# Kernel tuning notes

Hardware: AMD Instinct MI355X
Metric: run time of the kernel (lower is better)

The kernel has to match this reference:

```python
import jax, jax.numpy as jnp
import numpy as np

HIDDEN = 512


def setup_inputs() -> dict:
    key = jax.random.key(0)
    k_x, k_ih, k_hh = jax.random.split(key, 3)
    B, T, I, H = 128, 1000, 2, HIDDEN
    x = jax.random.uniform(k_x, (B, T, I), dtype=jnp.float32)
    s_ih = 1.0 / np.sqrt(I)
    s_hh = 1.0 / np.sqrt(H)
    weight_ih = jax.random.normal(k_ih, (I, 4 * H), dtype=jnp.float32) * s_ih
    weight_hh = jax.random.normal(k_hh, (H, 4 * H), dtype=jnp.float32) * s_hh
    bias = jnp.zeros((4 * H,), dtype=jnp.float32)
    return {"x": x, "weight_ih": weight_ih, "weight_hh": weight_hh, "bias": bias}


def _lstm(x, weight_ih, weight_hh, bias):
    # x: [B, T, I] (batch_first) -> scan over time
    B, T, I = x.shape
    H = weight_hh.shape[0]
    # Precompute input contribution for all timesteps: [T, B, 4H]
    x_t = jnp.transpose(x, (1, 0, 2))
    xW = jnp.einsum('tbi,ih->tbh', x_t, weight_ih) + bias

    def step(carry, xw_t):
        h0, c0 = carry
        gates = h0 @ weight_hh + xw_t  # [B, 4H]
        f, i, o, g = jnp.split(gates, 4, axis=1)
        c1 = jax.nn.sigmoid(f) * c0 + jax.nn.sigmoid(i) * jnp.tanh(g)
        h1 = jax.nn.sigmoid(o) * jnp.tanh(c1)
        return (h1, c1), (h1, c1)

    h0 = jnp.zeros((B, H), dtype=x.dtype)
    c0 = jnp.zeros((B, H), dtype=x.dtype)
    _, (h_n, c_n) = jax.lax.scan(step, (h0, c0), xW)
    # [T, B, H] -> [B, T, H] (batch_first)
    return jnp.transpose(h_n, (1, 0, 2)), jnp.transpose(c_n, (1, 0, 2))


def reference(x, weight_ih, weight_hh, bias):
    return _lstm(x, weight_ih, weight_hh, bias)
```

## Files before the change

### kernel.cpp

```cpp
#include <hip/hip_runtime.h>

#define TT 1000
#define HH 512
#define G4 2048
#define NG 32
#define SLOTS 8
#define SPG 4
#define HCBLK 64

typedef __attribute__((ext_vector_type(8))) short bf16x8;
typedef __attribute__((ext_vector_type(4))) float f32x4;

__device__ __forceinline__ float sigm(float v) { return 1.0f / (1.0f + __expf(-v)); }
__device__ __forceinline__ float tanh_fast(float v) { return 2.0f / (1.0f + __expf(-2.0f * v)) - 1.0f; }

__device__ __forceinline__ unsigned short bf16rne(float f) {
    unsigned u = __float_as_uint(f);
    return (unsigned short)((u + 0x7fffu + ((u >> 16) & 1u)) >> 16);
}

__global__ __launch_bounds__(512, 1)
void lstm_d8(const float* __restrict__ x,
             const float* __restrict__ wih,
             const float* __restrict__ whh,
             const float* __restrict__ bias,
             float* __restrict__ out,
             float* ws)
{
    __shared__ short hsh[16 * 512];

    const int bid  = blockIdx.x;
    const int g    = bid & (NG - 1);
    const int slot = bid >> 5;
    const int tid  = threadIdx.x;
    const int wv   = tid >> 6;
    const int lane = tid & 63;
    const int col  = lane & 15;
    const int kb   = lane >> 4;
    const int q    = col & 3;
    const int q1   = q & 1, q2 = q >> 1;
    const int cc   = col >> 2;
    const int rowSel = kb * 4 + q;
    const int row4   = rowSel & 3;
    const int bSel   = g * SPG + row4;
    const int hc0    = slot * HCBLK + wv * 8 + cc;
    const int hc1    = hc0 + 4;

    unsigned long long* slab = (unsigned long long*)ws;
    unsigned* flags = (unsigned*)((char*)ws + 256 * 1024);

    for (int i = tid; i < 4096; i += 512) ((unsigned*)hsh)[i] = 0u;

    const int gc0 = q * 512 + hc0;
    const int gc1 = q * 512 + hc1;
    bf16x8 breg0[16], breg1[16];
    #pragma unroll
    for (int kt = 0; kt < 16; ++kt) {
        bf16x8 f0, f1;
        #pragma unroll
        for (int j = 0; j < 8; ++j) {
            int k = kt * 32 + kb * 8 + j;
            f0[j] = (short)bf16rne(whh[(size_t)k * G4 + gc0]);
            f1[j] = (short)bf16rne(whh[(size_t)k * G4 + gc1]);
        }
        breg0[kt] = f0;
        breg1[kt] = f1;
    }

    float wA0[4], wB0[4], bb0[4], wA1[4], wB1[4], bb1[4];
    #pragma unroll
    for (int j = 0; j < 4; ++j) {
        int a0 = j * 512 + hc0, a1 = j * 512 + hc1;
        wA0[j] = wih[a0]; wB0[j] = wih[G4 + a0]; bb0[j] = bias[a0];
        wA1[j] = wih[a1]; wB1[j] = wih[G4 + a1]; bb1[j] = bias[a1];
    }

    const int arow = col;
    const int asw  = (arow & 7) << 3;
    const short* aBase = hsh + arow * 512;

    __syncthreads();

    float cst0 = 0.0f, cst1 = 0.0f;
    const size_t OSZ = (size_t)128 * TT * HH;
    const float* xp = x + (size_t)bSel * TT * 2;
    float2 xv = *(const float2*)(xp);

    for (int t = 0; t < TT; ++t) {
        f32x4 acc0 = {0.f, 0.f, 0.f, 0.f};
        f32x4 acc1 = {0.f, 0.f, 0.f, 0.f};
        #pragma unroll
        for (int kt = 0; kt < 16; ++kt) {
            int ka = kt * 32 + kb * 8;
            bf16x8 a = *(const bf16x8*)(aBase + (ka ^ asw));
            acc0 = __builtin_amdgcn_mfma_f32_16x16x32_bf16(a, breg0[kt], acc0, 0, 0, 0);
            acc1 = __builtin_amdgcn_mfma_f32_16x16x32_bf16(a, breg1[kt], acc1, 0, 0, 0);
        }

        float h1a, c1a;
        {
            float v0 = acc0[0], v1 = acc0[1], v2 = acc0[2], v3 = acc0[3];
            float vq = q2 ? (q1 ? v3 : v2) : (q1 ? v1 : v0);
            float s1 = q2 ? (q1 ? v2 : v3) : (q1 ? v0 : v1);
            float s2 = q2 ? (q1 ? v1 : v0) : (q1 ? v3 : v2);
            float s3 = q2 ? (q1 ? v0 : v1) : (q1 ? v2 : v3);
            float g1 = __shfl_xor(s1, 1);
            float g2 = __shfl_xor(s2, 2);
            float g3 = __shfl_xor(s3, 3);
            float fv = q2 ? (q1 ? g3 : g2) : (q1 ? g1 : vq);
            float iv = q2 ? (q1 ? g2 : g3) : (q1 ? vq : g1);
            float ov = q2 ? (q1 ? g1 : vq) : (q1 ? g3 : g2);
            float gv = q2 ? (q1 ? vq : g1) : (q1 ? g2 : g3);
            fv += xv.x * wA0[0] + xv.y * wB0[0] + bb0[0];
            iv += xv.x * wA0[1] + xv.y * wB0[1] + bb0[1];
            ov += xv.x * wA0[2] + xv.y * wB0[2] + bb0[2];
            gv += xv.x * wA0[3] + xv.y * wB0[3] + bb0[3];
            c1a = sigm(fv) * cst0 + sigm(iv) * tanh_fast(gv);
            h1a = sigm(ov) * tanh_fast(c1a);
            cst0 = c1a;
        }
        float h1b, c1b;
        {
            float v0 = acc1[0], v1 = acc1[1], v2 = acc1[2], v3 = acc1[3];
            float vq = q2 ? (q1 ? v3 : v2) : (q1 ? v1 : v0);
            float s1 = q2 ? (q1 ? v2 : v3) : (q1 ? v0 : v1);
            float s2 = q2 ? (q1 ? v1 : v0) : (q1 ? v3 : v2);
            float s3 = q2 ? (q1 ? v0 : v1) : (q1 ? v2 : v3);
            float g1 = __shfl_xor(s1, 1);
            float g2 = __shfl_xor(s2, 2);
            float g3 = __shfl_xor(s3, 3);
            float fv = q2 ? (q1 ? g3 : g2) : (q1 ? g1 : vq);
            float iv = q2 ? (q1 ? g2 : g3) : (q1 ? vq : g1);
            float ov = q2 ? (q1 ? g1 : vq) : (q1 ? g3 : g2);
            float gv = q2 ? (q1 ? vq : g1) : (q1 ? g2 : g3);
            fv += xv.x * wA1[0] + xv.y * wB1[0] + bb1[0];
            iv += xv.x * wA1[1] + xv.y * wB1[1] + bb1[1];
            ov += xv.x * wA1[2] + xv.y * wB1[2] + bb1[2];
            gv += xv.x * wA1[3] + xv.y * wB1[3] + bb1[3];
            c1b = sigm(fv) * cst1 + sigm(iv) * tanh_fast(gv);
            h1b = sigm(ov) * tanh_fast(c1b);
            cst1 = c1b;
        }

        float ha1 = __shfl_xor(h1a, 4), ha2 = __shfl_xor(h1a, 8), ha3 = __shfl_xor(ha1, 8);
        float hb1 = __shfl_xor(h1b, 4), hb2 = __shfl_xor(h1b, 8), hb3 = __shfl_xor(hb1, 8);
        float ca1 = __shfl_xor(c1a, 4), ca2 = __shfl_xor(c1a, 8), ca3 = __shfl_xor(ca1, 8);
        float cb1 = __shfl_xor(c1b, 4), cb2 = __shfl_xor(c1b, 8), cb3 = __shfl_xor(cb1, 8);

        const unsigned tag = (unsigned)(t + 1);
        const int phase = (t + 1) & 1;
        const int hbase0 = slot * HCBLK + wv * 8;
        const bool storer = (kb == 0) && (cc == 0);

        if (t + 1 < TT) {
            if (storer) {
                unsigned long long w0 =
                      (unsigned long long)bf16rne(h1a)
                    | ((unsigned long long)bf16rne(ha1) << 16)
                    | ((unsigned long long)bf16rne(ha2) << 32)
                    | ((unsigned long long)bf16rne(ha3) << 48);
                unsigned long long w1 =
                      (unsigned long long)bf16rne(h1b)
                    | ((unsigned long long)bf16rne(hb1) << 16)
                    | ((unsigned long long)bf16rne(hb2) << 32)
                    | ((unsigned long long)bf16rne(hb3) << 48);
                unsigned long long* dst = slab
                    + ((size_t)(phase * 128 + g * SPG + q)) * 128 + (hbase0 >> 2);
                __hip_atomic_store(dst,     w0, __ATOMIC_RELAXED, __HIP_MEMORY_SCOPE_AGENT);
                __hip_atomic_store(dst + 1, w1, __ATOMIC_RELAXED, __HIP_MEMORY_SCOPE_AGENT);
            }
            asm volatile("s_waitcnt vmcnt(0)" ::: "memory");
            __syncthreads();
            if (tid == 0)
                __hip_atomic_store(&flags[(g * SLOTS + slot) * 16], tag,
                                   __ATOMIC_RELAXED, __HIP_MEMORY_SCOPE_AGENT);
        }

        if (storer) {
            size_t oidx = ((size_t)(g * SPG + q) * TT + t) * HH + hbase0;
            float4 hq0 = {h1a, ha1, ha2, ha3};
            float4 cq0 = {c1a, ca1, ca2, ca3};
            float4 hq1 = {h1b, hb1, hb2, hb3};
            float4 cq1 = {c1b, cb1, cb2, cb3};
            *(float4*)(out + oidx) = hq0;
            *(float4*)(out + oidx + 4) = hq1;
            *(float4*)(out + OSZ + oidx) = cq0;
            *(float4*)(out + OSZ + oidx + 4) = cq1;
        }

        if (t + 1 < TT) {
            xv = *(const float2*)(xp + 2 * (t + 1));

            {
                long gd = 0;
                for (;;) {
                    unsigned fl = (lane < SLOTS)
                        ? __hip_atomic_load(&flags[(g * SLOTS + lane) * 16],
                                            __ATOMIC_RELAXED, __HIP_MEMORY_SCOPE_AGENT)
                        : tag;
                    if (__all(fl >= tag)) break;
                    __builtin_amdgcn_s_sleep(1);
                    if (++gd > 20000000L) break;
                }
            }

            {
                const unsigned long long* src = slab
                    + ((size_t)(phase * 128 + g * SPG)) * 128;
                unsigned long long d = __hip_atomic_load(src + tid,
                        __ATOMIC_RELAXED, __HIP_MEMORY_SCOPE_AGENT);
                int seq = tid >> 7;
                int k0  = (tid & 127) << 2;
                *(unsigned long long*)(hsh + seq * 512 + (k0 ^ ((seq & 7) << 3))) = d;
            }
            __syncthreads();
        }
    }
}

extern "C" void kernel_launch(void* const* d_in, const int* in_sizes, int n_in,
                              void* d_out, int out_size, void* d_ws, size_t ws_size,
                              hipStream_t stream) {
    const float* x    = (const float*)d_in[0];
    const float* wih  = (const float*)d_in[1];
    const float* whh  = (const float*)d_in[2];
    const float* bias = (const float*)d_in[3];
    float* out = (float*)d_out;
    float* ws  = (float*)d_ws;

    hipMemsetAsync((char*)d_ws + 256 * 1024, 0, NG * SLOTS * 16 * sizeof(unsigned), stream);

    dim3 grid(NG * SLOTS), block(512);
    hipLaunchKernelGGL(lstm_d8, grid, block, 0, stream, x, wih, whh, bias, out, ws);
}
```

Baseline: 3.028 ms.

## Embed step tags in bf16 payload bits and sync per-wave without flags

Replaces the per-block flag array and block-wide barriers with tag bits carried in the bf16 exponent-MSB positions of each 64-bit h payload. Each wave independently polls the slab for its group's h values until the tags match, then strips them and writes them into a private per-wave LDS buffer. This removes the store-then-flag round trip, the vmcnt wait and both __syncthreads per step. The MFMA A operand now only loads the 4 real rows (lanes col<4) instead of 16 padded rows. The scheme assumes bit 14 of every bf16 h value is zero, which holds for |h|<2 because tanh bounds h. Every wave now redundantly reads the whole group slab, which raises global polling traffic.

```diff
diff --git a/kernel.cpp b/kernel.cpp
--- a/kernel.cpp
+++ b/kernel.cpp
@@ -20,14 +20,14 @@
 }
 
 __global__ __launch_bounds__(512, 1)
-void lstm_d8(const float* __restrict__ x,
+void lstm_wf(const float* __restrict__ x,
              const float* __restrict__ wih,
              const float* __restrict__ whh,
              const float* __restrict__ bias,
              float* __restrict__ out,
              float* ws)
 {
-    __shared__ short hsh[16 * 512];
+    __shared__ unsigned long long lds64[8][4][132];
 
     const int bid  = blockIdx.x;
     const int g    = bid & (NG - 1);
@@ -40,16 +40,14 @@
     const int q    = col & 3;
     const int q1   = q & 1, q2 = q >> 1;
     const int cc   = col >> 2;
-    const int rowSel = kb * 4 + q;
-    const int row4   = rowSel & 3;
-    const int bSel   = g * SPG + row4;
-    const int hc0    = slot * HCBLK + wv * 8 + cc;
-    const int hc1    = hc0 + 4;
+    const int hc0  = slot * HCBLK + wv * 8 + cc;
+    const int hc1  = hc0 + 4;
 
     unsigned long long* slab = (unsigned long long*)ws;
-    unsigned* flags = (unsigned*)((char*)ws + 256 * 1024);
-
-    for (int i = tid; i < 4096; i += 512) ((unsigned*)hsh)[i] = 0u;
+    const unsigned long long TAGM = 0x4000400040004000ULL;
+
+    for (int i = lane; i < 4 * 132; i += 64)
+        ((unsigned long long*)lds64[wv])[i] = 0ULL;
 
     const int gc0 = q * 512 + hc0;
     const int gc1 = q * 512 + hc1;
@@ -75,24 +73,21 @@
         wA1[j] = wih[a1]; wB1[j] = wih[G4 + a1]; bb1[j] = bias[a1];
     }
 
-    const int arow = col;
-    const int asw  = (arow & 7) << 3;
-    const short* aBase = hsh + arow * 512;
-
-    __syncthreads();
-
     float cst0 = 0.0f, cst1 = 0.0f;
     const size_t OSZ = (size_t)128 * TT * HH;
+    const int bSel = g * SPG + q;
     const float* xp = x + (size_t)bSel * TT * 2;
     float2 xv = *(const float2*)(xp);
+    const bool storer = (kb == 0) && (cc == 0);
 
     for (int t = 0; t < TT; ++t) {
         f32x4 acc0 = {0.f, 0.f, 0.f, 0.f};
         f32x4 acc1 = {0.f, 0.f, 0.f, 0.f};
         #pragma unroll
         for (int kt = 0; kt < 16; ++kt) {
-            int ka = kt * 32 + kb * 8;
-            bf16x8 a = *(const bf16x8*)(aBase + (ka ^ asw));
+            bf16x8 a = {0, 0, 0, 0, 0, 0, 0, 0};
+            if (col < 4)
+                a = *(const bf16x8*)&lds64[wv][col][(kt * 8 + kb * 2) ^ (2 * col)];
             acc0 = __builtin_amdgcn_mfma_f32_16x16x32_bf16(a, breg0[kt], acc0, 0, 0, 0);
             acc1 = __builtin_amdgcn_mfma_f32_16x16x32_bf16(a, breg1[kt], acc1, 0, 0, 0);
         }
@@ -147,37 +142,33 @@
         float ca1 = __shfl_xor(c1a, 4), ca2 = __shfl_xor(c1a, 8), ca3 = __shfl_xor(ca1, 8);
         float cb1 = __shfl_xor(c1b, 4), cb2 = __shfl_xor(c1b, 8), cb3 = __shfl_xor(cb1, 8);
 
-        const unsigned tag = (unsigned)(t + 1);
+        const unsigned tag4 = (unsigned)(t + 1) & 15u;
         const int phase = (t + 1) & 1;
-        const int hbase0 = slot * HCBLK + wv * 8;
-        const bool storer = (kb == 0) && (cc == 0);
-
-        if (t + 1 < TT) {
-            if (storer) {
-                unsigned long long w0 =
-                      (unsigned long long)bf16rne(h1a)
-                    | ((unsigned long long)bf16rne(ha1) << 16)
-                    | ((unsigned long long)bf16rne(ha2) << 32)
-                    | ((unsigned long long)bf16rne(ha3) << 48);
-                unsigned long long w1 =
-                      (unsigned long long)bf16rne(h1b)
-                    | ((unsigned long long)bf16rne(hb1) << 16)
-                    | ((unsigned long long)bf16rne(hb2) << 32)
-                    | ((unsigned long long)bf16rne(hb3) << 48);
-                unsigned long long* dst = slab
-                    + ((size_t)(phase * 128 + g * SPG + q)) * 128 + (hbase0 >> 2);
-                __hip_atomic_store(dst,     w0, __ATOMIC_RELAXED, __HIP_MEMORY_SCOPE_AGENT);
-                __hip_atomic_store(dst + 1, w1, __ATOMIC_RELAXED, __HIP_MEMORY_SCOPE_AGENT);
-            }
-            asm volatile("s_waitcnt vmcnt(0)" ::: "memory");
-            __syncthreads();
-            if (tid == 0)
-                __hip_atomic_store(&flags[(g * SLOTS + slot) * 16], tag,
-                                   __ATOMIC_RELAXED, __HIP_MEMORY_SCOPE_AGENT);
+        const unsigned long long tpat =
+              ((unsigned long long)(tag4 & 1u)        << 14)
+            | ((unsigned long long)((tag4 >> 1) & 1u) << 30)
+            | ((unsigned long long)((tag4 >> 2) & 1u) << 46)
+            | ((unsigned long long)((tag4 >> 3) & 1u) << 62);
+
+        if (t + 1 < TT && storer) {
+            unsigned long long w0 =
+                  (unsigned long long)bf16rne(h1a)
+                | ((unsigned long long)bf16rne(ha1) << 16)
+                | ((unsigned long long)bf16rne(ha2) << 32)
+                | ((unsigned long long)bf16rne(ha3) << 48) | tpat;
+            unsigned long long w1 =
+                  (unsigned long long)bf16rne(h1b)
+                | ((unsigned long long)bf16rne(hb1) << 16)
+                | ((unsigned long long)bf16rne(hb2) << 32)
+                | ((unsigned long long)bf16rne(hb3) << 48) | tpat;
+            unsigned long long* dst = slab
+                + ((size_t)(phase * 128 + bSel)) * 128 + slot * 16 + wv * 2;
+            __hip_atomic_store(dst,     w0, __ATOMIC_RELAXED, __HIP_MEMORY_SCOPE_AGENT);
+            __hip_atomic_store(dst + 1, w1, __ATOMIC_RELAXED, __HIP_MEMORY_SCOPE_AGENT);
         }
 
         if (storer) {
-            size_t oidx = ((size_t)(g * SPG + q) * TT + t) * HH + hbase0;
+            size_t oidx = ((size_t)bSel * TT + t) * HH + slot * HCBLK + wv * 8;
             float4 hq0 = {h1a, ha1, ha2, ha3};
             float4 cq0 = {c1a, ca1, ca2, ca3};
             float4 hq1 = {h1b, hb1, hb2, hb3};
@@ -191,29 +182,35 @@
         if (t + 1 < TT) {
             xv = *(const float2*)(xp + 2 * (t + 1));
 
-            {
-                long gd = 0;
-                for (;;) {
-                    unsigned fl = (lane < SLOTS)
-                        ? __hip_atomic_load(&flags[(g * SLOTS + lane) * 16],
-                                            __ATOMIC_RELAXED, __HIP_MEMORY_SCOPE_AGENT)
-                        : tag;
-                    if (__all(fl >= tag)) break;
-                    __builtin_amdgcn_s_sleep(1);
-                    if (++gd > 20000000L) break;
+            const unsigned long long* src = slab
+                + ((size_t)(phase * 128 + g * SPG)) * 128;
+            unsigned long long vals[8];
+            #pragma unroll
+            for (int j = 0; j < 8; ++j)
+                vals[j] = __hip_atomic_load(src + j * 64 + lane,
+                              __ATOMIC_RELAXED, __HIP_MEMORY_SCOPE_AGENT);
+            unsigned pend = 0u;
+            #pragma unroll
+            for (int j = 0; j < 8; ++j)
+                if ((vals[j] & TAGM) != tpat) pend |= (1u << j);
+
+            long gd = 0;
+            while (pend) {
+                __builtin_amdgcn_s_sleep(1);
+                #pragma unroll
+                for (int j = 0; j < 8; ++j) if (pend & (1u << j)) {
+                    unsigned long long v = __hip_atomic_load(src + j * 64 + lane,
+                            __ATOMIC_RELAXED, __HIP_MEMORY_SCOPE_AGENT);
+                    if ((v & TAGM) == tpat) { vals[j] = v; pend &= ~(1u << j); }
                 }
+                if (++gd > 20000000L) break;
             }
 
-            {
-                const unsigned long long* src = slab
-                    + ((size_t)(phase * 128 + g * SPG)) * 128;
-                unsigned long long d = __hip_atomic_load(src + tid,
-                        __ATOMIC_RELAXED, __HIP_MEMORY_SCOPE_AGENT);
-                int seq = tid >> 7;
-                int k0  = (tid & 127) << 2;
-                *(unsigned long long*)(hsh + seq * 512 + (k0 ^ ((seq & 7) << 3))) = d;
+            #pragma unroll
+            for (int j = 0; j < 8; ++j) {
+                const int row = j >> 1;
+                lds64[wv][row][(((j & 1) * 64 + lane) ^ (2 * row))] = vals[j] & ~TAGM;
             }
-            __syncthreads();
         }
     }
 }
@@ -228,8 +225,8 @@
     float* out = (float*)d_out;
     float* ws  = (float*)d_ws;
 
-    hipMemsetAsync((char*)d_ws + 256 * 1024, 0, NG * SLOTS * 16 * sizeof(unsigned), stream);
+    hipMemsetAsync(d_ws, 0, 2 * 128 * 128 * sizeof(unsigned long long), stream);
 
     dim3 grid(NG * SLOTS), block(512);
-    hipLaunchKernelGGL(lstm_d8, grid, block, 0, stream, x, wih, whh, bias, out, ws);
+    hipLaunchKernelGGL(lstm_wf, grid, block, 0, stream, x, wih, whh, bias, out, ws);
 }
```

After: 10.65 ms. +251.7%, slower.
